# Optimization experiments

Measured on AMD Instinct MI355X. Metric: run time of the kernel, lower is better.

## Reference

```python
import jax, jax.numpy as jnp
import numpy as np

B, N, E = 8, 4096, 131072
F_IN, F_OUT = 64, 64
ALPHA = 0.2  # LeakyReLU negative slope


def setup_inputs() -> dict:
    key = jax.random.key(0)
    k1, k2, k3, k4, k5 = jax.random.split(key, 5)
    h = jax.random.normal(k1, (B, N, F_IN), dtype=jnp.float32)
    edge_index = jax.random.randint(k2, (2, E), 0, N)
    edge_weight = jax.random.uniform(k3, (E,), dtype=jnp.float32)
    # learned params: Linear weight (no bias) and attention vector a (2*F_OUT, 1)
    W = jax.random.normal(k4, (F_IN, F_OUT), dtype=jnp.float32) / np.sqrt(F_IN)
    a = jax.random.normal(k5, (2 * F_OUT, 1), dtype=jnp.float32) * 0.1
    return {"h": h, "edge_index": edge_index, "edge_weight": edge_weight, "W": W, "a": a}


def _gat_forward(h, edge_weight, W, a, src, dst):
    # Wh: (B, N, F')
    Wh = jnp.einsum("bnf,fo->bno", h, W)
    a1, a2 = a[:F_OUT, 0], a[F_OUT:, 0]
    # score decomposition: [Wh_src || Wh_dst] @ a == Wh_src@a1 + Wh_dst@a2
    s_src = Wh @ a1  # (B, N)
    s_dst = Wh @ a2  # (B, N)
    e = s_src[:, src] + s_dst[:, dst]           # (B, E)
    e = jnp.where(e > 0, e, ALPHA * e)          # LeakyReLU
    e = e * edge_weight[None, :]
    # sparse row-softmax over dst, grouped by src (equals dense masked softmax)
    eT = e.T                                     # (E, B)
    m = jax.ops.segment_max(eT, src, num_segments=N)   # (N, B)
    m = jnp.where(jnp.isfinite(m), m, 0.0)       # rows with no edges
    ex = jnp.exp(eT - m[src])                    # (E, B)
    denom = jax.ops.segment_sum(ex, src, num_segments=N)  # (N, B)
    attn = ex / denom[src]                       # (E, B); denom>0 wherever an edge exists
    # aggregate: h'[b, i] = sum_{e: src[e]=i} attn[e,b] * Wh[b, dst[e]]
    msg = attn[:, :, None] * jnp.transpose(Wh[:, dst], (1, 0, 2))  # (E, B, F')
    hp = jax.ops.segment_sum(msg, src, num_segments=N)             # (N, B, F')
    hp = jnp.transpose(hp, (1, 0, 2))            # (B, N, F')
    return jnp.where(hp > 0, hp, jnp.expm1(hp))  # ELU


def reference(h, edge_index, edge_weight, W, a):
    src, dst = edge_index[0], edge_index[1]
    return _gat_forward(h, edge_weight, W, a, src, dst)
```

## Files before the change

### kernel.cpp

```cpp
#include <hip/hip_runtime.h>
#include <math.h>

#define NB 8
#define NN 4096
#define NE 131072
#define NF 64
#define CAP 256
#define PCAP 128
#define LRELU_ALPHA 0.2f

static __device__ __forceinline__ ushort bf16r(float x) {
  uint u = __float_as_uint(x);
  return (ushort)((u + 0x7fffu + ((u >> 16) & 1u)) >> 16);
}

__global__ __launch_bounds__(256) void fused_gemm_append_kernel(
    const float* __restrict__ h, const float* __restrict__ W,
    const float* __restrict__ a, const int* __restrict__ src,
    const int* __restrict__ dst, const float* __restrict__ ew,
    ushort* __restrict__ Whb, float* __restrict__ ssrc,
    float* __restrict__ sdst, int* __restrict__ cnt,
    int2* __restrict__ bucket) {
  int tid = threadIdx.x;
  int blk = blockIdx.x;
  if (blk >= 512) {
    int e = (blk - 512) * 256 + tid;
    int s = src[e];
    int d = dst[e];
    float w = ew[e];
    int p = atomicAdd(&cnt[s], 1);
    if (p < CAP) bucket[s * CAP + p] = make_int2(d, __float_as_int(w));
    return;
  }
  int f = tid & 63;
  int wave = blk * 4 + (tid >> 6);
  float Wc[64];
#pragma unroll
  for (int k = 0; k < 64; k++) Wc[k] = W[k * 64 + f];
  float A1 = a[f];
  float A2 = a[64 + f];

  int row0 = __builtin_amdgcn_readfirstlane(wave) * 16;
#pragma unroll 2
  for (int r = 0; r < 16; r++) {
    int row = row0 + r;
    const float* hr = h + (size_t)row * NF;
    float ac0 = 0.f, ac1 = 0.f, ac2 = 0.f, ac3 = 0.f;
#pragma unroll
    for (int k = 0; k < 64; k += 4) {
      ac0 += hr[k] * Wc[k];
      ac1 += hr[k + 1] * Wc[k + 1];
      ac2 += hr[k + 2] * Wc[k + 2];
      ac3 += hr[k + 3] * Wc[k + 3];
    }
    float acc = (ac0 + ac1) + (ac2 + ac3);
    Whb[(size_t)row * NF + f] = bf16r(acc);
    float v1 = acc * A1;
    float v2 = acc * A2;
#pragma unroll
    for (int off = 1; off < 64; off <<= 1) {
      v1 += __shfl_xor(v1, off);
      v2 += __shfl_xor(v2, off);
    }
    if (f == 0) ssrc[row] = v1;
    if (f == 32) sdst[row] = v2;
  }
}

__global__ __launch_bounds__(512) void agg_kernel(
    const ushort* __restrict__ Whb, const float* __restrict__ ssrc,
    const float* __restrict__ sdst, const int* __restrict__ cnt,
    const int2* __restrict__ bucket, float* __restrict__ out) {
  __shared__ int2 pex[8][PCAP];
  int blk = blockIdx.x;
  int b = blk & 7;
  int g = blk >> 3;
  int tid = threadIdx.x;
  int w = tid >> 6;
  int f = tid & 63;
  int n = g * 8 + w;

  int cntn = min(cnt[n], PCAP);
  float ss = ssrc[b * NN + n];
  const float* sdB = sdst + b * NN;
  const int2* bkt = bucket + n * CAP;
  float den = 0.f;
  for (int i = f; i < cntn; i += 64) {
    int2 e = bkt[i];
    float x = ss + sdB[e.x];
    x = (x > 0.f) ? x : LRELU_ALPHA * x;
    x *= __int_as_float(e.y);
    float v = __expf(x);
    pex[w][i] = make_int2(e.x, __float_as_int(v));
    den += v;
  }
#pragma unroll
  for (int off = 1; off < 64; off <<= 1) den += __shfl_xor(den, off);

  const ushort* WhB = Whb + (size_t)b * NN * NF;
  const int4* pv = (const int4*)&pex[w][0];
  float acc0 = 0.f, acc1 = 0.f, acc2 = 0.f, acc3 = 0.f;
  float acc4 = 0.f, acc5 = 0.f, acc6 = 0.f, acc7 = 0.f;
  int i = 0;
  for (; i + 8 <= cntn; i += 8) {
    int4 q0 = pv[(i >> 1) + 0];
    int4 q1 = pv[(i >> 1) + 1];
    int4 q2 = pv[(i >> 1) + 2];
    int4 q3 = pv[(i >> 1) + 3];
    float w0 = __uint_as_float(((uint)WhB[(q0.x << 6) + f]) << 16);
    float w1 = __uint_as_float(((uint)WhB[(q0.z << 6) + f]) << 16);
    float w2 = __uint_as_float(((uint)WhB[(q1.x << 6) + f]) << 16);
    float w3 = __uint_as_float(((uint)WhB[(q1.z << 6) + f]) << 16);
    float w4 = __uint_as_float(((uint)WhB[(q2.x << 6) + f]) << 16);
    float w5 = __uint_as_float(((uint)WhB[(q2.z << 6) + f]) << 16);
    float w6 = __uint_as_float(((uint)WhB[(q3.x << 6) + f]) << 16);
    float w7 = __uint_as_float(((uint)WhB[(q3.z << 6) + f]) << 16);
    acc0 += __int_as_float(q0.y) * w0;
    acc1 += __int_as_float(q0.w) * w1;
    acc2 += __int_as_float(q1.y) * w2;
    acc3 += __int_as_float(q1.w) * w3;
    acc4 += __int_as_float(q2.y) * w4;
    acc5 += __int_as_float(q2.w) * w5;
    acc6 += __int_as_float(q3.y) * w6;
    acc7 += __int_as_float(q3.w) * w7;
  }
  for (; i < cntn; i++) {
    int2 p = pex[w][i];
    acc0 += __int_as_float(p.y) *
            __uint_as_float(((uint)WhB[(p.x << 6) + f]) << 16);
  }
  float accs = ((acc0 + acc1) + (acc2 + acc3)) + ((acc4 + acc5) + (acc6 + acc7));
  float hp = (cntn > 0) ? accs / den : 0.f;
  out[((size_t)(b * NN + n)) * NF + f] = (hp > 0.f) ? hp : expm1f(hp);
}

extern "C" void kernel_launch(void* const* d_in, const int* in_sizes, int n_in,
                              void* d_out, int out_size, void* d_ws,
                              size_t ws_size, hipStream_t stream) {
  const float* h = (const float*)d_in[0];
  const int* edge_index = (const int*)d_in[1];
  const float* ew = (const float*)d_in[2];
  const float* W = (const float*)d_in[3];
  const float* a = (const float*)d_in[4];
  float* out = (float*)d_out;

  const int* src = edge_index;
  const int* dst = edge_index + NE;

  uint8_t* ws = (uint8_t*)d_ws;
  ushort* Whb = (ushort*)ws;
  float* ssrc = (float*)(ws + 4194304);
  float* sdst = (float*)(ws + 4325376);
  int* cnt = (int*)(ws + 4456448);
  int2* bucket = (int2*)(ws + 4472832);

  hipMemsetAsync(cnt, 0, NN * sizeof(int), stream);
  fused_gemm_append_kernel<<<1024, 256, 0, stream>>>(h, W, a, src, dst, ew,
                                                     Whb, ssrc, sdst, cnt,
                                                     bucket);
  agg_kernel<<<NN, 512, 0, stream>>>(Whb, ssrc, sdst, cnt, bucket, out);
}
```

Measured before the change: 118.2 us.

## Fuse memset, GEMM, bucketing and aggregation into one cooperative persistent kernel

```diff
diff --git a/kernel.cpp b/kernel.cpp
--- a/kernel.cpp
+++ b/kernel.cpp
@@ -1,5 +1,8 @@
 #include <hip/hip_runtime.h>
+#include <hip/hip_cooperative_groups.h>
 #include <math.h>
+
+namespace cg = cooperative_groups;
 
 #define NB 8
 #define NN 4096
@@ -14,124 +17,127 @@
   return (ushort)((u + 0x7fffu + ((u >> 16) & 1u)) >> 16);
 }
 
-__global__ __launch_bounds__(256) void fused_gemm_append_kernel(
+__global__ __launch_bounds__(256, 2) void gat_fused_kernel(
     const float* __restrict__ h, const float* __restrict__ W,
     const float* __restrict__ a, const int* __restrict__ src,
     const int* __restrict__ dst, const float* __restrict__ ew,
     ushort* __restrict__ Whb, float* __restrict__ ssrc,
     float* __restrict__ sdst, int* __restrict__ cnt,
-    int2* __restrict__ bucket) {
+    int2* __restrict__ bucket, float* __restrict__ out) {
+  cg::grid_group grid = cg::this_grid();
+  __shared__ int2 pex[4][PCAP];
   int tid = threadIdx.x;
   int blk = blockIdx.x;
-  if (blk >= 512) {
-    int e = (blk - 512) * 256 + tid;
+  int f = tid & 63;
+  int w = tid >> 6;
+
+  if (tid < 8) cnt[blk * 8 + tid] = 0;
+  __threadfence();
+  grid.sync();
+
+  {
+    float Wc[64];
+#pragma unroll
+    for (int k = 0; k < 64; k++) Wc[k] = W[k * 64 + f];
+    float A1 = a[f];
+    float A2 = a[64 + f];
+    int row0 = __builtin_amdgcn_readfirstlane(blk * 4 + w) * 16;
+#pragma unroll 2
+    for (int r = 0; r < 16; r++) {
+      int row = row0 + r;
+      const float* hr = h + (size_t)row * NF;
+      float ac0 = 0.f, ac1 = 0.f, ac2 = 0.f, ac3 = 0.f;
+#pragma unroll
+      for (int k = 0; k < 64; k += 4) {
+        ac0 += hr[k] * Wc[k];
+        ac1 += hr[k + 1] * Wc[k + 1];
+        ac2 += hr[k + 2] * Wc[k + 2];
+        ac3 += hr[k + 3] * Wc[k + 3];
+      }
+      float acc = (ac0 + ac1) + (ac2 + ac3);
+      Whb[(size_t)row * NF + f] = bf16r(acc);
+      float v1 = acc * A1;
+      float v2 = acc * A2;
+#pragma unroll
+      for (int off = 1; off < 64; off <<= 1) {
+        v1 += __shfl_xor(v1, off);
+        v2 += __shfl_xor(v2, off);
+      }
+      if (f == 0) ssrc[row] = v1;
+      if (f == 32) sdst[row] = v2;
+    }
+  }
+  {
+    int e = blk * 256 + tid;
     int s = src[e];
     int d = dst[e];
-    float w = ew[e];
+    float wt = ew[e];
     int p = atomicAdd(&cnt[s], 1);
-    if (p < CAP) bucket[s * CAP + p] = make_int2(d, __float_as_int(w));
-    return;
+    if (p < CAP) bucket[s * CAP + p] = make_int2(d, __float_as_int(wt));
   }
-  int f = tid & 63;
-  int wave = blk * 4 + (tid >> 6);
-  float Wc[64];
+  __threadfence();
+  grid.sync();
+
+  {
+    int b = blk & 7;
+    int j = blk >> 3;
+    const float* sdB = sdst + b * NN;
+    const ushort* WhB = Whb + (size_t)b * NN * NF;
+    for (int it = 0; it < 16; it++) {
+      int n = j * 64 + it * 4 + w;
+      int cntn = min(cnt[n], PCAP);
+      float ss = ssrc[b * NN + n];
+      const int2* bkt = bucket + n * CAP;
+      float den = 0.f;
+      for (int i = f; i < cntn; i += 64) {
+        int2 e = bkt[i];
+        float x = ss + sdB[e.x];
+        x = (x > 0.f) ? x : LRELU_ALPHA * x;
+        x *= __int_as_float(e.y);
+        float v = __expf(x);
+        pex[w][i] = make_int2(e.x, __float_as_int(v));
+        den += v;
+      }
 #pragma unroll
-  for (int k = 0; k < 64; k++) Wc[k] = W[k * 64 + f];
-  float A1 = a[f];
-  float A2 = a[64 + f];
+      for (int off = 1; off < 64; off <<= 1) den += __shfl_xor(den, off);
 
-  int row0 = __builtin_amdgcn_readfirstlane(wave) * 16;
-#pragma unroll 2
-  for (int r = 0; r < 16; r++) {
-    int row = row0 + r;
-    const float* hr = h + (size_t)row * NF;
-    float ac0 = 0.f, ac1 = 0.f, ac2 = 0.f, ac3 = 0.f;
-#pragma unroll
-    for (int k = 0; k < 64; k += 4) {
-      ac0 += hr[k] * Wc[k];
-      ac1 += hr[k + 1] * Wc[k + 1];
-      ac2 += hr[k + 2] * Wc[k + 2];
-      ac3 += hr[k + 3] * Wc[k + 3];
+      const int4* pv = (const int4*)&pex[w][0];
+      float acc0 = 0.f, acc1 = 0.f, acc2 = 0.f, acc3 = 0.f;
+      float acc4 = 0.f, acc5 = 0.f, acc6 = 0.f, acc7 = 0.f;
+      int i = 0;
+      for (; i + 8 <= cntn; i += 8) {
+        int4 q0 = pv[(i >> 1) + 0];
+        int4 q1 = pv[(i >> 1) + 1];
+        int4 q2 = pv[(i >> 1) + 2];
+        int4 q3 = pv[(i >> 1) + 3];
+        float w0 = __uint_as_float(((uint)WhB[(q0.x << 6) + f]) << 16);
+        float w1 = __uint_as_float(((uint)WhB[(q0.z << 6) + f]) << 16);
+        float w2 = __uint_as_float(((uint)WhB[(q1.x << 6) + f]) << 16);
+        float w3 = __uint_as_float(((uint)WhB[(q1.z << 6) + f]) << 16);
+        float w4 = __uint_as_float(((uint)WhB[(q2.x << 6) + f]) << 16);
+        float w5 = __uint_as_float(((uint)WhB[(q2.z << 6) + f]) << 16);
+        float w6 = __uint_as_float(((uint)WhB[(q3.x << 6) + f]) << 16);
+        float w7 = __uint_as_float(((uint)WhB[(q3.z << 6) + f]) << 16);
+        acc0 += __int_as_float(q0.y) * w0;
+        acc1 += __int_as_float(q0.w) * w1;
+        acc2 += __int_as_float(q1.y) * w2;
+        acc3 += __int_as_float(q1.w) * w3;
+        acc4 += __int_as_float(q2.y) * w4;
+        acc5 += __int_as_float(q2.w) * w5;
+        acc6 += __int_as_float(q3.y) * w6;
+        acc7 += __int_as_float(q3.w) * w7;
+      }
+      for (; i < cntn; i++) {
+        int2 p = pex[w][i];
+        acc0 += __int_as_float(p.y) *
+                __uint_as_float(((uint)WhB[(p.x << 6) + f]) << 16);
+      }
+      float accs =
+          ((acc0 + acc1) + (acc2 + acc3)) + ((acc4 + acc5) + (acc6 + acc7));
+      float hp = (cntn > 0) ? accs / den : 0.f;
+      out[((size_t)(b * NN + n)) * NF + f] = (hp > 0.f) ? hp : expm1f(hp);
     }
-    float acc = (ac0 + ac1) + (ac2 + ac3);
-    Whb[(size_t)row * NF + f] = bf16r(acc);
-    float v1 = acc * A1;
-    float v2 = acc * A2;
-#pragma unroll
-    for (int off = 1; off < 64; off <<= 1) {
-      v1 += __shfl_xor(v1, off);
-      v2 += __shfl_xor(v2, off);
-    }
-    if (f == 0) ssrc[row] = v1;
-    if (f == 32) sdst[row] = v2;
   }
-}
-
-__global__ __launch_bounds__(512) void agg_kernel(
-    const ushort* __restrict__ Whb, const float* __restrict__ ssrc,
-    const float* __restrict__ sdst, const int* __restrict__ cnt,
-    const int2* __restrict__ bucket, float* __restrict__ out) {
-  __shared__ int2 pex[8][PCAP];
-  int blk = blockIdx.x;
-  int b = blk & 7;
-  int g = blk >> 3;
-  int tid = threadIdx.x;
-  int w = tid >> 6;
-  int f = tid & 63;
-  int n = g * 8 + w;
-
-  int cntn = min(cnt[n], PCAP);
-  float ss = ssrc[b * NN + n];
-  const float* sdB = sdst + b * NN;
-  const int2* bkt = bucket + n * CAP;
-  float den = 0.f;
-  for (int i = f; i < cntn; i += 64) {
-    int2 e = bkt[i];
-    float x = ss + sdB[e.x];
-    x = (x > 0.f) ? x : LRELU_ALPHA * x;
-    x *= __int_as_float(e.y);
-    float v = __expf(x);
-    pex[w][i] = make_int2(e.x, __float_as_int(v));
-    den += v;
-  }
-#pragma unroll
-  for (int off = 1; off < 64; off <<= 1) den += __shfl_xor(den, off);
-
-  const ushort* WhB = Whb + (size_t)b * NN * NF;
-  const int4* pv = (const int4*)&pex[w][0];
-  float acc0 = 0.f, acc1 = 0.f, acc2 = 0.f, acc3 = 0.f;
-  float acc4 = 0.f, acc5 = 0.f, acc6 = 0.f, acc7 = 0.f;
-  int i = 0;
-  for (; i + 8 <= cntn; i += 8) {
-    int4 q0 = pv[(i >> 1) + 0];
-    int4 q1 = pv[(i >> 1) + 1];
-    int4 q2 = pv[(i >> 1) + 2];
-    int4 q3 = pv[(i >> 1) + 3];
-    float w0 = __uint_as_float(((uint)WhB[(q0.x << 6) + f]) << 16);
-    float w1 = __uint_as_float(((uint)WhB[(q0.z << 6) + f]) << 16);
-    float w2 = __uint_as_float(((uint)WhB[(q1.x << 6) + f]) << 16);
-    float w3 = __uint_as_float(((uint)WhB[(q1.z << 6) + f]) << 16);
-    float w4 = __uint_as_float(((uint)WhB[(q2.x << 6) + f]) << 16);
-    float w5 = __uint_as_float(((uint)WhB[(q2.z << 6) + f]) << 16);
-    float w6 = __uint_as_float(((uint)WhB[(q3.x << 6) + f]) << 16);
-    float w7 = __uint_as_float(((uint)WhB[(q3.z << 6) + f]) << 16);
-    acc0 += __int_as_float(q0.y) * w0;
-    acc1 += __int_as_float(q0.w) * w1;
-    acc2 += __int_as_float(q1.y) * w2;
-    acc3 += __int_as_float(q1.w) * w3;
-    acc4 += __int_as_float(q2.y) * w4;
-    acc5 += __int_as_float(q2.w) * w5;
-    acc6 += __int_as_float(q3.y) * w6;
-    acc7 += __int_as_float(q3.w) * w7;
-  }
-  for (; i < cntn; i++) {
-    int2 p = pex[w][i];
-    acc0 += __int_as_float(p.y) *
-            __uint_as_float(((uint)WhB[(p.x << 6) + f]) << 16);
-  }
-  float accs = ((acc0 + acc1) + (acc2 + acc3)) + ((acc4 + acc5) + (acc6 + acc7));
-  float hp = (cntn > 0) ? accs / den : 0.f;
-  out[((size_t)(b * NN + n)) * NF + f] = (hp > 0.f) ? hp : expm1f(hp);
 }
 
 extern "C" void kernel_launch(void* const* d_in, const int* in_sizes, int n_in,
@@ -154,9 +160,9 @@
   int* cnt = (int*)(ws + 4456448);
   int2* bucket = (int2*)(ws + 4472832);
 
-  hipMemsetAsync(cnt, 0, NN * sizeof(int), stream);
-  fused_gemm_append_kernel<<<1024, 256, 0, stream>>>(h, W, a, src, dst, ew,
-                                                     Whb, ssrc, sdst, cnt,
-                                                     bucket);
-  agg_kernel<<<NN, 512, 0, stream>>>(Whb, ssrc, sdst, cnt, bucket, out);
+  void* args[] = {(void*)&h,    (void*)&W,    (void*)&a,   (void*)&src,
+                  (void*)&dst,  (void*)&ew,   (void*)&Whb, (void*)&ssrc,
+                  (void*)&sdst, (void*)&cnt,  (void*)&bucket, (void*)&out};
+  hipLaunchCooperativeKernel((void*)gat_fused_kernel, dim3(512), dim3(256),
+                             args, 0, stream);
 }
```

Measured after the change: 321.8 us. 172% more time.
